# Kernel optimization log

Hardware: AMD Instinct MI355X
Metric: run time of the kernel (lower is better)

Reference implementation:

```python
import jax, jax.numpy as jnp
import numpy as np

N_EMBD = 768
N_HEAD = 12
N_KV_HEAD = 4                      # repeat factor in _repeat_kv
NUM_KV_HEADS = N_HEAD // N_KV_HEAD # 3 actual kv heads
HEAD_DIM = N_EMBD // N_HEAD        # 64
BLOCK_SIZE = 1024                  # sliding window size
SCALE = (HEAD_DIM * N_KV_HEAD / N_HEAD) ** (-0.5)


def _rotary_cos_sin(T, d, dtype):
    inv_freq = 1.0 / (10000.0 ** (jnp.arange(0, d, 2, dtype=jnp.float32) / d))
    t = jnp.arange(T, dtype=jnp.float32)
    freqs = jnp.outer(t, inv_freq)  # (T, d/2)
    return jnp.cos(freqs).astype(dtype)[None, None], jnp.sin(freqs).astype(dtype)[None, None]


def _apply_rotary(x):
    # x: (b, h, T, d)
    T, d = x.shape[2], x.shape[3]
    cos, sin = _rotary_cos_sin(T, d, x.dtype)
    x1, x2 = x[..., : d // 2], x[..., d // 2 :]
    return jnp.concatenate([x1 * cos - x2 * sin, x1 * sin + x2 * cos], axis=-1)


def setup_inputs() -> dict:
    key = jax.random.key(0)
    k0, k1, k2, k3, k4 = jax.random.split(key, 5)
    b, T = 2, 2048
    s = 0.02
    return {
        "hidden_states": jax.random.normal(k0, (b, T, N_EMBD), jnp.float32),
        "Wq": jax.random.normal(k1, (N_HEAD * HEAD_DIM, N_EMBD), jnp.float32) * s,
        "Wk": jax.random.normal(k2, (NUM_KV_HEADS * HEAD_DIM, N_EMBD), jnp.float32) * s,
        "Wv": jax.random.normal(k3, (NUM_KV_HEADS * HEAD_DIM, N_EMBD), jnp.float32) * s,
        "Wo": jax.random.normal(k4, (N_EMBD, N_HEAD * HEAD_DIM), jnp.float32) * s,
    }


def reference(hidden_states, Wq, Wk, Wv, Wo):
    b, T, _ = hidden_states.shape
    q = (hidden_states @ Wq.T).reshape(b, T, N_HEAD, HEAD_DIM).transpose(0, 2, 1, 3)
    k = (hidden_states @ Wk.T).reshape(b, T, NUM_KV_HEADS, HEAD_DIM).transpose(0, 2, 1, 3)
    v = (hidden_states @ Wv.T).reshape(b, T, NUM_KV_HEADS, HEAD_DIM).transpose(0, 2, 1, 3)

    # _repeat_kv: each kv head repeated n_kv_head (=4) times contiguously
    k = jnp.repeat(k, N_KV_HEAD, axis=1)
    v = jnp.repeat(v, N_KV_HEAD, axis=1)

    q = _apply_rotary(q)
    k = _apply_rotary(k)

    # centered sliding-window mask (faithful to per-token loop):
    # window_start = clip(i - W//2, 0, T - W); window is always exactly W wide
    W = BLOCK_SIZE
    i = jnp.arange(T)[:, None]
    j = jnp.arange(T)[None, :]
    start = jnp.clip(i - W // 2, 0, T - W)
    mask = (j >= start) & (j < start + W)  # (T, T)

    scores = jnp.einsum("bhqd,bhkd->bhqk", q, k) * SCALE
    scores = jnp.where(mask[None, None], scores, jnp.finfo(scores.dtype).min)
    attn = jax.nn.softmax(scores, axis=-1)
    out = jnp.einsum("bhqk,bhkd->bhqd", attn, v)  # (b, h, T, d)

    out = out.transpose(0, 2, 1, 3).reshape(b, T, N_EMBD)
    return out @ Wo.T
```

## Files before the change

### kernel.cpp

```cpp
#include <hip/hip_runtime.h>
#include <math.h>

#define T_SEQ 2048
#define E 768
#define WIN 1024
#define KDIM 768
#define HS_SZ ((size_t)4096 * 768)
#define SCALE 0.21650635094610965f

typedef _Float16 f16x8 __attribute__((ext_vector_type(8)));
typedef _Float16 f16x4 __attribute__((ext_vector_type(4)));
typedef float f32x4 __attribute__((ext_vector_type(4)));
typedef __attribute__((address_space(3))) _Float16 lf16;

#define MFMA16(a, b, c) __builtin_amdgcn_mfma_f32_16x16x32_f16(a, b, c, 0, 0, 0)

__device__ __forceinline__ void dma16(const _Float16* g, lf16* l) {
    __builtin_amdgcn_global_load_lds(
        (const __attribute__((address_space(1))) void*)g,
        (__attribute__((address_space(3))) void*)l, 16, 0, 0);
}

__device__ __forceinline__ void cast8(const float* __restrict__ src,
                                      _Float16* __restrict__ dst, int i) {
    float4 a = *(const float4*)&src[i];
    float4 b = *(const float4*)&src[i + 4];
    f16x8 h;
    h[0] = (_Float16)a.x; h[1] = (_Float16)a.y; h[2] = (_Float16)a.z; h[3] = (_Float16)a.w;
    h[4] = (_Float16)b.x; h[5] = (_Float16)b.y; h[6] = (_Float16)b.z; h[7] = (_Float16)b.w;
    *(f16x8*)&dst[i] = h;
}

__global__ __launch_bounds__(256) void prep(
    const float* __restrict__ hs,
    const float* __restrict__ Wq, const float* __restrict__ Wk,
    const float* __restrict__ Wv, const float* __restrict__ Wo,
    _Float16* __restrict__ hs16,
    _Float16* __restrict__ Wq16, _Float16* __restrict__ Wk16,
    _Float16* __restrict__ Wv16, _Float16* __restrict__ Wo16,
    float2* __restrict__ rtab) {
    int tid = blockIdx.x * 256 + threadIdx.x;
    int i = tid * 8;
    if (i < 768 * 768) { cast8(Wq, Wq16, i); cast8(Wo, Wo16, i); }
    if (i < 192 * 768) { cast8(Wk, Wk16, i); cast8(Wv, Wv16, i); }
    cast8(hs, hs16, i);
    if (tid < 2048 * 32) {
        int t = tid >> 5, d = tid & 31;
        float inv = powf(10000.0f, -(float)(2 * d) * (1.0f / 64.0f));
        float s, c;
        sincosf((float)t * inv, &s, &c);
        rtab[tid] = make_float2(c, s);
    }
}

__global__ __launch_bounds__(256) void gemm_qkv(
    const _Float16* __restrict__ A16,
    const _Float16* __restrict__ Wq16, const _Float16* __restrict__ Wk16,
    const _Float16* __restrict__ Wv16, const float2* __restrict__ rtab,
    _Float16* __restrict__ q16, _Float16* __restrict__ k16,
    _Float16* __restrict__ vT16) {
    __shared__ __align__(16) _Float16 As[128 * 128];
    __shared__ __align__(16) _Float16 Bs[64 * 128];
    const int tid = threadIdx.x;
    const int bx = blockIdx.x;
    const int m0 = blockIdx.y * 128;
    const int w = tid >> 6, lane = tid & 63;
    const int mm = lane & 15, quad = lane >> 4;

    const _Float16* bbase; int brb;
    if (bx < 12)      { bbase = Wq16; brb = bx * 64; }
    else if (bx < 15) { bbase = Wk16; brb = (bx - 12) * 64; }
    else              { bbase = Wv16; brb = (bx - 15) * 64; }

    const int rofs4 = lane >> 4;
    const int gs = lane & 15;

    const _Float16* agp[8]; lf16* alp[8];
    #pragma unroll
    for (int j = 0; j < 8; ++j) {
        int c = j * 4 + w;
        int rr = c * 4 + rofs4;
        int glog = gs ^ (rr & 15);
        agp[j] = A16 + (size_t)(m0 + rr) * KDIM + glog * 8;
        alp[j] = ((lf16*)As) + c * 512 + lane * 8;
    }
    const _Float16* bgp[4]; lf16* blp[4];
    #pragma unroll
    for (int j = 0; j < 4; ++j) {
        int c = j * 4 + w;
        int rr = c * 4 + rofs4;
        int glog = gs ^ (rr & 15);
        bgp[j] = bbase + (size_t)(brb + rr) * KDIM + glog * 8;
        blp[j] = ((lf16*)Bs) + c * 512 + lane * 8;
    }

    f32x4 acc[2][4] = {};

    for (int it = 0; it < 6; ++it) {
        const int ke = it * 128;
        __syncthreads();
        #pragma unroll
        for (int j = 0; j < 8; ++j) dma16(agp[j] + ke, alp[j]);
        #pragma unroll
        for (int j = 0; j < 4; ++j) dma16(bgp[j] + ke, blp[j]);
        __syncthreads();
        #pragma unroll
        for (int s = 0; s < 4; ++s) {
            const int gq = ((s * 4 + quad) ^ mm) * 8;
            f16x8 ah[2];
            #pragma unroll
            for (int mt = 0; mt < 2; ++mt)
                ah[mt] = *(const f16x8*)&As[(w * 32 + mt * 16 + mm) * 128 + gq];
            #pragma unroll
            for (int nt = 0; nt < 4; ++nt) {
                f16x8 bh = *(const f16x8*)&Bs[(nt * 16 + mm) * 128 + gq];
                #pragma unroll
                for (int mt = 0; mt < 2; ++mt)
                    acc[mt][nt] = MFMA16(ah[mt], bh, acc[mt][nt]);
            }
        }
    }

    #pragma unroll
    for (int mt = 0; mt < 2; ++mt) {
        #pragma unroll
        for (int r = 0; r < 4; ++r) {
            int row = m0 + w * 32 + mt * 16 + quad * 4 + r;
            int t = row & (T_SEQ - 1);
            int b = row >> 11;
            if (bx < 12) {
                _Float16* dst = &q16[(size_t)row * E + bx * 64 + mm];
                #pragma unroll
                for (int nt = 0; nt < 2; ++nt) {
                    int d = nt * 16 + mm;
                    float2 cs = rtab[t * 32 + d];
                    float x1 = acc[mt][nt][r], x2 = acc[mt][nt + 2][r];
                    dst[nt * 16]       = (_Float16)((x1 * cs.x - x2 * cs.y) * SCALE);
                    dst[(nt + 2) * 16] = (_Float16)((x1 * cs.y + x2 * cs.x) * SCALE);
                }
            } else if (bx < 15) {
                int kvh = bx - 12;
                _Float16* dst = &k16[(((size_t)(b * 3 + kvh)) * T_SEQ + t) * 64 + mm];
                #pragma unroll
                for (int nt = 0; nt < 2; ++nt) {
                    int d = nt * 16 + mm;
                    float2 cs = rtab[t * 32 + d];
                    float x1 = acc[mt][nt][r], x2 = acc[mt][nt + 2][r];
                    dst[nt * 16]       = (_Float16)(x1 * cs.x - x2 * cs.y);
                    dst[(nt + 2) * 16] = (_Float16)(x1 * cs.y + x2 * cs.x);
                }
            } else {
                int kvh = bx - 15;
                #pragma unroll
                for (int nt = 0; nt < 4; ++nt) {
                    int d = nt * 16 + mm;
                    vT16[(((size_t)(b * 3 + kvh)) * 64 + d) * T_SEQ + t] = (_Float16)acc[mt][nt][r];
                }
            }
        }
    }
}

__global__ __launch_bounds__(256) void gemm_out(
    const _Float16* __restrict__ A16, const _Float16* __restrict__ B16,
    float* __restrict__ C) {
    __shared__ __align__(16) _Float16 As[64 * 128];
    __shared__ __align__(16) _Float16 Bs[64 * 128];
    const int tid = threadIdx.x;
    const int n0 = blockIdx.x * 64;
    const int m0 = blockIdx.y * 64;
    const int w = tid >> 6, lane = tid & 63;
    const int mm = lane & 15, quad = lane >> 4;
    const int wm = (w & 1) * 32, wn = (w >> 1) * 32;

    const int rofs4 = lane >> 4;
    const int gs = lane & 15;

    const _Float16* agp[4]; lf16* alp[4];
    const _Float16* bgp[4]; lf16* blp[4];
    #pragma unroll
    for (int j = 0; j < 4; ++j) {
        int c = j * 4 + w;
        int rr = c * 4 + rofs4;
        int glog = gs ^ (rr & 15);
        agp[j] = A16 + (size_t)(m0 + rr) * KDIM + glog * 8;
        alp[j] = ((lf16*)As) + c * 512 + lane * 8;
        bgp[j] = B16 + (size_t)(n0 + rr) * KDIM + glog * 8;
        blp[j] = ((lf16*)Bs) + c * 512 + lane * 8;
    }

    f32x4 acc[2][2] = {};

    for (int it = 0; it < 6; ++it) {
        const int ke = it * 128;
        __syncthreads();
        #pragma unroll
        for (int j = 0; j < 4; ++j) dma16(agp[j] + ke, alp[j]);
        #pragma unroll
        for (int j = 0; j < 4; ++j) dma16(bgp[j] + ke, blp[j]);
        __syncthreads();
        #pragma unroll
        for (int s = 0; s < 4; ++s) {
            const int gq = ((s * 4 + quad) ^ mm) * 8;
            f16x8 ah[2], bh[2];
            #pragma unroll
            for (int mt = 0; mt < 2; ++mt)
                ah[mt] = *(const f16x8*)&As[(wm + mt * 16 + mm) * 128 + gq];
            #pragma unroll
            for (int nt = 0; nt < 2; ++nt)
                bh[nt] = *(const f16x8*)&Bs[(wn + nt * 16 + mm) * 128 + gq];
            #pragma unroll
            for (int nt = 0; nt < 2; ++nt)
                #pragma unroll
                for (int mt = 0; mt < 2; ++mt)
                    acc[mt][nt] = MFMA16(ah[mt], bh[nt], acc[mt][nt]);
        }
    }
    #pragma unroll
    for (int mt = 0; mt < 2; ++mt)
        #pragma unroll
        for (int r = 0; r < 4; ++r) {
            int row = m0 + wm + mt * 16 + quad * 4 + r;
            float* cp = &C[(size_t)row * 768 + n0 + wn + mm];
            #pragma unroll
            for (int nt = 0; nt < 2; ++nt)
                cp[nt * 16] = acc[mt][nt][r];
        }
}

__global__ __launch_bounds__(256) void attn_mfma(const _Float16* __restrict__ q16,
                                                 const _Float16* __restrict__ k16,
                                                 const _Float16* __restrict__ vT16,
                                                 _Float16* __restrict__ aout16) {
    __shared__ __align__(16) char smem[8192 + 8192 + 10240];
    _Float16* k_s  = (_Float16*)smem;
    _Float16* vT_s = (_Float16*)(smem + 8192);
    _Float16 (*p_s)[40] = (_Float16(*)[40])(smem + 16384);
    float* ored = (float*)smem;
    float* lred = (float*)(smem + 16384);

    const int b = blockIdx.z, h = blockIdx.y;
    const int i0 = blockIdx.x * 64;
    const int plane = b * 3 + (h >> 2);
    const int tid = threadIdx.x;
    const int w = tid >> 6, lane = tid & 63;
    const int m = lane & 15, quad = lane >> 4;
    const int qh = w & 1, kh = w >> 1;
    const int xm = m & 7;

    int s0 = i0 - 512;      s0 = s0 < 0 ? 0 : (s0 > 1024 ? 1024 : s0);
    int sL = i0 + 63 - 512; sL = sL < 0 ? 0 : (sL > 1024 ? 1024 : sL);
    const int nc = (sL + WIN - s0 + 63) >> 6;

    int start_q[2];
    f16x8 qf[2][2];
    #pragma unroll
    for (int qt = 0; qt < 2; ++qt) {
        int qi = i0 + qh * 32 + qt * 16 + m;
        int sq = qi - 512; sq = sq < 0 ? 0 : (sq > 1024 ? 1024 : sq);
        start_q[qt] = sq;
        const _Float16* qp = &q16[((size_t)(b * T_SEQ + qi)) * E + h * 64 + quad * 8];
        qf[qt][0] = *(const f16x8*)&qp[0];
        qf[qt][1] = *(const f16x8*)&qp[32];
    }

    f32x4 o[2][4] = {};
    float l_run[2] = {0.0f, 0.0f};

    const int rofs = lane >> 3;
    const int glog = (lane & 7) ^ rofs;
    const _Float16* kgb[2]; const _Float16* vgb[2];
    _Float16* klw[2]; _Float16* vlw[2];
    #pragma unroll
    for (int j = 0; j < 2; ++j) {
        int rr = (j * 4 + w) * 8 + rofs;
        kgb[j] = k16 + ((size_t)plane * T_SEQ + rr) * 64 + glog * 8;
        vgb[j] = vT16 + ((size_t)plane * 64 + rr) * T_SEQ + glog * 8;
        klw[j] = k_s + (j * 4 + w) * 512 + lane * 8;
        vlw[j] = vT_s + (j * 4 + w) * 512 + lane * 8;
    }

    f16x8 kr[2], vr[2];
    #pragma unroll
    for (int j = 0; j < 2; ++j) {
        kr[j] = *(const f16x8*)(kgb[j] + (size_t)s0 * 64);
        vr[j] = *(const f16x8*)(vgb[j] + s0);
    }

    for (int ci = 0; ci < nc; ++ci) {
        const int c0 = s0 + ci * 64;
        __syncthreads();
        #pragma unroll
        for (int j = 0; j < 2; ++j) {
            *(f16x8*)klw[j] = kr[j];
            *(f16x8*)vlw[j] = vr[j];
        }
        __syncthreads();
        if (ci + 1 < nc) {
            const int cn = c0 + 64;
            #pragma unroll
            for (int j = 0; j < 2; ++j) {
                kr[j] = *(const f16x8*)(kgb[j] + (size_t)cn * 64);
                vr[j] = *(const f16x8*)(vgb[j] + cn);
            }
        }

        f32x4 st[2][2] = {};
        #pragma unroll
        for (int s = 0; s < 2; ++s) {
            #pragma unroll
            for (int kt = 0; kt < 2; ++kt) {
                int row = kh * 32 + kt * 16 + m;
                int g = (s * 4 + quad) ^ xm;
                f16x8 a = *(const f16x8*)&k_s[row * 64 + g * 8];
                #pragma unroll
                for (int qt = 0; qt < 2; ++qt)
                    st[kt][qt] = MFMA16(a, qf[qt][s], st[kt][qt]);
            }
        }

        const bool boundary = (c0 < sL) || (c0 + 63 > s0 + 1023);
        if (boundary) {
            #pragma unroll
            for (int kt = 0; kt < 2; ++kt)
                #pragma unroll
                for (int qt = 0; qt < 2; ++qt)
                    #pragma unroll
                    for (int r = 0; r < 4; ++r) {
                        int j = c0 + kh * 32 + kt * 16 + quad * 4 + r;
                        bool valid = (j >= start_q[qt]) && (j < start_q[qt] + WIN);
                        st[kt][qt][r] = valid ? st[kt][qt][r] : -INFINITY;
                    }
        }

        #pragma unroll
        for (int kt = 0; kt < 2; ++kt)
            #pragma unroll
            for (int qt = 0; qt < 2; ++qt) {
                float p0 = __expf(st[kt][qt][0]);
                float p1 = __expf(st[kt][qt][1]);
                float p2 = __expf(st[kt][qt][2]);
                float p3 = __expf(st[kt][qt][3]);
                l_run[qt] += (p0 + p1) + (p2 + p3);
                f16x4 pv = {(_Float16)p0, (_Float16)p1, (_Float16)p2, (_Float16)p3};
                *(f16x4*)&p_s[w * 32 + qt * 16 + m][kt * 16 + quad * 4] = pv;
            }

        f16x8 bp[2];
        #pragma unroll
        for (int qt = 0; qt < 2; ++qt)
            bp[qt] = *(const f16x8*)&p_s[w * 32 + qt * 16 + m][quad * 8];
        #pragma unroll
        for (int mt = 0; mt < 4; ++mt) {
            int g = (kh * 4 + quad) ^ xm;
            f16x8 a = *(const f16x8*)&vT_s[(mt * 16 + m) * 64 + g * 8];
            #pragma unroll
            for (int qt = 0; qt < 2; ++qt)
                o[qt][mt] = MFMA16(a, bp[qt], o[qt][mt]);
        }
    }

    float l_tot[2];
    #pragma unroll
    for (int qt = 0; qt < 2; ++qt) {
        float l = l_run[qt];
        l += __shfl_xor(l, 16);
        l += __shfl_xor(l, 32);
        l_tot[qt] = l;
    }

    __syncthreads();
    if (kh == 1) {
        #pragma unroll
        for (int qt = 0; qt < 2; ++qt) {
            #pragma unroll
            for (int mt = 0; mt < 4; ++mt) {
                int idx = ((qh * 32 + qt * 16 + m) << 6) + mt * 16 + quad * 4;
                *(float4*)&ored[idx] = *(float4*)&o[qt][mt];
            }
            if (quad == 0) lred[qh * 32 + qt * 16 + m] = l_tot[qt];
        }
    }
    __syncthreads();
    if (kh == 0) {
        #pragma unroll
        for (int qt = 0; qt < 2; ++qt) {
            float rl = 1.0f / (l_tot[qt] + lred[qh * 32 + qt * 16 + m]);
            int qi = i0 + qh * 32 + qt * 16 + m;
            _Float16* op = &aout16[((size_t)(b * T_SEQ + qi)) * E + h * 64];
            #pragma unroll
            for (int mt = 0; mt < 4; ++mt) {
                int idx = ((qh * 32 + qt * 16 + m) << 6) + mt * 16 + quad * 4;
                float4 other = *(float4*)&ored[idx];
                #pragma unroll
                for (int r = 0; r < 4; ++r) {
                    float x = (o[qt][mt][r] + (&other.x)[r]) * rl;
                    op[mt * 16 + quad * 4 + r] = (_Float16)x;
                }
            }
        }
    }
}

extern "C" void kernel_launch(void* const* d_in, const int* in_sizes, int n_in,
                              void* d_out, int out_size, void* d_ws, size_t ws_size,
                              hipStream_t stream) {
    const float* hs = (const float*)d_in[0];
    const float* Wq = (const float*)d_in[1];
    const float* Wk = (const float*)d_in[2];
    const float* Wv = (const float*)d_in[3];
    const float* Wo = (const float*)d_in[4];
    float* out = (float*)d_out;

    _Float16* hs16   = (_Float16*)d_ws;
    _Float16* aout16 = hs16 + HS_SZ;
    _Float16* q16    = aout16 + HS_SZ;
    _Float16* k16    = q16 + HS_SZ;
    _Float16* vT16   = k16 + 6 * 2048 * 64;
    _Float16* Wq16   = vT16 + 6 * 2048 * 64;
    _Float16* Wk16   = Wq16 + 768 * 768;
    _Float16* Wv16   = Wk16 + 192 * 768;
    _Float16* Wo16   = Wv16 + 192 * 768;
    float2*   rtab   = (float2*)(Wo16 + 768 * 768);

    dim3 blk(256);
    prep<<<dim3((int)(HS_SZ / 8 / 256)), blk, 0, stream>>>(hs, Wq, Wk, Wv, Wo,
                                                           hs16, Wq16, Wk16, Wv16, Wo16, rtab);
    gemm_qkv<<<dim3(18, 32), blk, 0, stream>>>(hs16, Wq16, Wk16, Wv16, rtab, q16, k16, vT16);
    attn_mfma<<<dim3(32, 12, 2), blk, 0, stream>>>(q16, k16, vT16, aout16);
    gemm_out<<<dim3(12, 64), blk, 0, stream>>>(aout16, Wo16, out);
}
```

Measured before the change: 135.3 us.

## Stage 128-key K/V chunks into LDS via direct global-to-LDS DMA

The attention loop now stages K and V^T tiles covering 128 keys per barrier pair instead of 64, halving the number of __syncthreads per window. Loads go straight from global memory to LDS with global_load_lds instead of a register prefetch plus an LDS store. The V^T layout changes to a 128-wide row with a 16-way XOR swizzle. The loads are no longer overlapped with compute, because the register double-buffering is removed, and the larger LDS footprint may reduce occupancy.

```diff
diff --git a/kernel.cpp b/kernel.cpp
--- a/kernel.cpp
+++ b/kernel.cpp
@@ -232,10 +232,10 @@
                                                  const _Float16* __restrict__ k16,
                                                  const _Float16* __restrict__ vT16,
                                                  _Float16* __restrict__ aout16) {
-    __shared__ __align__(16) char smem[8192 + 8192 + 10240];
+    __shared__ __align__(16) char smem[16384 + 16384 + 10240];
     _Float16* k_s  = (_Float16*)smem;
-    _Float16* vT_s = (_Float16*)(smem + 8192);
-    _Float16 (*p_s)[40] = (_Float16(*)[40])(smem + 16384);
+    _Float16* vT_s = (_Float16*)(smem + 16384);
+    _Float16 (*p_s)[40] = (_Float16(*)[40])(smem + 32768);
     float* ored = (float*)smem;
     float* lred = (float*)(smem + 16384);
 
@@ -251,6 +251,7 @@
     int s0 = i0 - 512;      s0 = s0 < 0 ? 0 : (s0 > 1024 ? 1024 : s0);
     int sL = i0 + 63 - 512; sL = sL < 0 ? 0 : (sL > 1024 ? 1024 : sL);
     const int nc = (sL + WIN - s0 + 63) >> 6;
+    const int ndc = (nc + 1) >> 1;
 
     int start_q[2];
     f16x8 qf[2][2];
@@ -267,96 +268,93 @@
     f32x4 o[2][4] = {};
     float l_run[2] = {0.0f, 0.0f};
 
-    const int rofs = lane >> 3;
-    const int glog = (lane & 7) ^ rofs;
-    const _Float16* kgb[2]; const _Float16* vgb[2];
-    _Float16* klw[2]; _Float16* vlw[2];
-    #pragma unroll
-    for (int j = 0; j < 2; ++j) {
-        int rr = (j * 4 + w) * 8 + rofs;
-        kgb[j] = k16 + ((size_t)plane * T_SEQ + rr) * 64 + glog * 8;
+    const int rofs8 = lane >> 3;
+    const int glog8 = (lane & 7) ^ rofs8;
+    const _Float16* kgb[4]; lf16* klw[4];
+    #pragma unroll
+    for (int j = 0; j < 4; ++j) {
+        int rr = (j * 4 + w) * 8 + rofs8;
+        kgb[j] = k16 + ((size_t)plane * T_SEQ + rr) * 64 + glog8 * 8;
+        klw[j] = ((lf16*)k_s) + (j * 4 + w) * 512 + lane * 8;
+    }
+    const int rofs4 = lane >> 4;
+    const int gs = lane & 15;
+    const _Float16* vgb[4]; lf16* vlw[4];
+    #pragma unroll
+    for (int j = 0; j < 4; ++j) {
+        int rr = (j * 4 + w) * 4 + rofs4;
+        int glog = gs ^ (rr & 15);
         vgb[j] = vT16 + ((size_t)plane * 64 + rr) * T_SEQ + glog * 8;
-        klw[j] = k_s + (j * 4 + w) * 512 + lane * 8;
-        vlw[j] = vT_s + (j * 4 + w) * 512 + lane * 8;
-    }
-
-    f16x8 kr[2], vr[2];
-    #pragma unroll
-    for (int j = 0; j < 2; ++j) {
-        kr[j] = *(const f16x8*)(kgb[j] + (size_t)s0 * 64);
-        vr[j] = *(const f16x8*)(vgb[j] + s0);
-    }
-
-    for (int ci = 0; ci < nc; ++ci) {
-        const int c0 = s0 + ci * 64;
-        __syncthreads();
-        #pragma unroll
-        for (int j = 0; j < 2; ++j) {
-            *(f16x8*)klw[j] = kr[j];
-            *(f16x8*)vlw[j] = vr[j];
-        }
-        __syncthreads();
-        if (ci + 1 < nc) {
-            const int cn = c0 + 64;
-            #pragma unroll
-            for (int j = 0; j < 2; ++j) {
-                kr[j] = *(const f16x8*)(kgb[j] + (size_t)cn * 64);
-                vr[j] = *(const f16x8*)(vgb[j] + cn);
-            }
-        }
-
-        f32x4 st[2][2] = {};
-        #pragma unroll
-        for (int s = 0; s < 2; ++s) {
-            #pragma unroll
-            for (int kt = 0; kt < 2; ++kt) {
-                int row = kh * 32 + kt * 16 + m;
-                int g = (s * 4 + quad) ^ xm;
-                f16x8 a = *(const f16x8*)&k_s[row * 64 + g * 8];
+        vlw[j] = ((lf16*)vT_s) + (j * 4 + w) * 512 + lane * 8;
+    }
+
+    for (int ci = 0; ci < ndc; ++ci) {
+        const int c0 = s0 + ci * 128;
+        __syncthreads();
+        #pragma unroll
+        for (int j = 0; j < 4; ++j) dma16(kgb[j] + (size_t)c0 * 64, klw[j]);
+        #pragma unroll
+        for (int j = 0; j < 4; ++j) dma16(vgb[j] + c0, vlw[j]);
+        __syncthreads();
+
+        #pragma unroll
+        for (int sc = 0; sc < 2; ++sc) {
+            if (ci * 2 + sc >= nc) break;
+            const int c0s = c0 + sc * 64;
+
+            f32x4 st[2][2] = {};
+            #pragma unroll
+            for (int s = 0; s < 2; ++s) {
+                #pragma unroll
+                for (int kt = 0; kt < 2; ++kt) {
+                    int row = sc * 64 + kh * 32 + kt * 16 + m;
+                    int g = (s * 4 + quad) ^ xm;
+                    f16x8 a = *(const f16x8*)&k_s[row * 64 + g * 8];
+                    #pragma unroll
+                    for (int qt = 0; qt < 2; ++qt)
+                        st[kt][qt] = MFMA16(a, qf[qt][s], st[kt][qt]);
+                }
+            }
+
+            const bool boundary = (c0s < sL) || (c0s + 63 > s0 + 1023);
+            if (boundary) {
+                #pragma unroll
+                for (int kt = 0; kt < 2; ++kt)
+                    #pragma unroll
+                    for (int qt = 0; qt < 2; ++qt)
+                        #pragma unroll
+                        for (int r = 0; r < 4; ++r) {
+                            int j = c0s + kh * 32 + kt * 16 + quad * 4 + r;
+                            bool valid = (j >= start_q[qt]) && (j < start_q[qt] + WIN);
+                            st[kt][qt][r] = valid ? st[kt][qt][r] : -INFINITY;
+                        }
+            }
+
+            #pragma unroll
+            for (int kt = 0; kt < 2; ++kt)
+                #pragma unroll
+                for (int qt = 0; qt < 2; ++qt) {
+                    float p0 = __expf(st[kt][qt][0]);
+                    float p1 = __expf(st[kt][qt][1]);
+                    float p2 = __expf(st[kt][qt][2]);
+                    float p3 = __expf(st[kt][qt][3]);
+                    l_run[qt] += (p0 + p1) + (p2 + p3);
+                    f16x4 pv = {(_Float16)p0, (_Float16)p1, (_Float16)p2, (_Float16)p3};
+                    *(f16x4*)&p_s[w * 32 + qt * 16 + m][kt * 16 + quad * 4] = pv;
+                }
+
+            f16x8 bp[2];
+            #pragma unroll
+            for (int qt = 0; qt < 2; ++qt)
+                bp[qt] = *(const f16x8*)&p_s[w * 32 + qt * 16 + m][quad * 8];
+            #pragma unroll
+            for (int mt = 0; mt < 4; ++mt) {
+                int g = (sc * 8 + kh * 4 + quad) ^ m;
+                f16x8 a = *(const f16x8*)&vT_s[(mt * 16 + m) * 128 + g * 8];
                 #pragma unroll
                 for (int qt = 0; qt < 2; ++qt)
-                    st[kt][qt] = MFMA16(a, qf[qt][s], st[kt][qt]);
-            }
-        }
-
-        const bool boundary = (c0 < sL) || (c0 + 63 > s0 + 1023);
-        if (boundary) {
-            #pragma unroll
-            for (int kt = 0; kt < 2; ++kt)
-                #pragma unroll
-                for (int qt = 0; qt < 2; ++qt)
-                    #pragma unroll
-                    for (int r = 0; r < 4; ++r) {
-                        int j = c0 + kh * 32 + kt * 16 + quad * 4 + r;
-                        bool valid = (j >= start_q[qt]) && (j < start_q[qt] + WIN);
-                        st[kt][qt][r] = valid ? st[kt][qt][r] : -INFINITY;
-                    }
-        }
-
-        #pragma unroll
-        for (int kt = 0; kt < 2; ++kt)
-            #pragma unroll
-            for (int qt = 0; qt < 2; ++qt) {
-                float p0 = __expf(st[kt][qt][0]);
-                float p1 = __expf(st[kt][qt][1]);
-                float p2 = __expf(st[kt][qt][2]);
-                float p3 = __expf(st[kt][qt][3]);
-                l_run[qt] += (p0 + p1) + (p2 + p3);
-                f16x4 pv = {(_Float16)p0, (_Float16)p1, (_Float16)p2, (_Float16)p3};
-                *(f16x4*)&p_s[w * 32 + qt * 16 + m][kt * 16 + quad * 4] = pv;
-            }
-
-        f16x8 bp[2];
-        #pragma unroll
-        for (int qt = 0; qt < 2; ++qt)
-            bp[qt] = *(const f16x8*)&p_s[w * 32 + qt * 16 + m][quad * 8];
-        #pragma unroll
-        for (int mt = 0; mt < 4; ++mt) {
-            int g = (kh * 4 + quad) ^ xm;
-            f16x8 a = *(const f16x8*)&vT_s[(mt * 16 + m) * 64 + g * 8];
-            #pragma unroll
-            for (int qt = 0; qt < 2; ++qt)
-                o[qt][mt] = MFMA16(a, bp[qt], o[qt][mt]);
+                    o[qt][mt] = MFMA16(a, bp[qt], o[qt][mt]);
+            }
         }
     }
 
```

Result: slower. 142.2 us (+5.1%).
